# Kernel tuning notes

Hardware: AMD Instinct MI355X
Metric: run time of the kernel (lower is better)

The kernel has to match this reference:

```python
import jax, jax.numpy as jnp
import numpy as np

N = 50000
E = 800000
NODE_IN = 128
HID = 256
OUT = 256
EDGE_DIM = 16
HEADS = 4
CH = HID // HEADS  # 64
NEG_SLOPE = 0.2


def _init_linear(key, fan_in, fan_out):
    k1, k2 = jax.random.split(key)
    bound = 1.0 / np.sqrt(fan_in)
    W = jax.random.uniform(k1, (fan_in, fan_out), jnp.float32, -bound, bound)
    b = jax.random.uniform(k2, (fan_out,), jnp.float32, -bound, bound)
    return W, b


def setup_inputs() -> dict:
    key = jax.random.key(0)
    ks = jax.random.split(key, 12)
    node_feats = jax.random.normal(ks[0], (N, NODE_IN), jnp.float32)
    edge_index = jax.random.randint(ks[1], (2, E), 0, N, jnp.int64)
    edge_attr = jax.random.normal(ks[2], (E, EDGE_DIM), jnp.float32)

    Wnp, bnp = _init_linear(ks[3], NODE_IN, HID)           # node_proj
    Wep, bep = _init_linear(ks[4], EDGE_DIM, HID)          # edge_proj
    # GATConv 1: in = 2*HID, out per head = CH
    Wg1, _ = _init_linear(ks[5], 2 * HID, HEADS * CH)
    as1 = jax.random.normal(ks[6], (HEADS, CH), jnp.float32) * 0.1
    ad1 = jax.random.normal(ks[7], (HEADS, CH), jnp.float32) * 0.1
    bg1 = jnp.zeros((HEADS * CH,), jnp.float32)
    # GATConv 2: in = HID, out per head = OUT//HEADS
    Wg2, _ = _init_linear(ks[8], HID, HEADS * (OUT // HEADS))
    as2 = jax.random.normal(ks[9], (HEADS, OUT // HEADS), jnp.float32) * 0.1
    ad2 = jax.random.normal(ks[10], (HEADS, OUT // HEADS), jnp.float32) * 0.1
    bg2 = jnp.zeros((OUT,), jnp.float32)
    Wo, bo = _init_linear(ks[11], OUT, OUT)                # out_proj
    return {
        "node_feats": node_feats, "edge_attr": edge_attr,
        "Wnp": Wnp, "bnp": bnp, "Wep": Wep, "bep": bep,
        "Wg1": Wg1, "as1": as1, "ad1": ad1, "bg1": bg1,
        "Wg2": Wg2, "as2": as2, "ad2": ad2, "bg2": bg2,
        "Wo": Wo, "bo": bo,
        "edge_index": edge_index,
    }


def scatter_mean(src, index, num_nodes):
    # mean of edge features grouped by target node; empty groups -> 0 (count clamped to 1)
    s = jax.ops.segment_sum(src, index, num_segments=num_nodes)
    cnt = jax.ops.segment_sum(jnp.ones((src.shape[0],), src.dtype), index, num_segments=num_nodes)
    return s / jnp.maximum(cnt, 1.0)[:, None]


def gat_conv(x, src, dst, W, att_src, att_dst, bias, num_nodes, heads, ch):
    # PyG GATConv with add_self_loops=True (loops appended by caller via src/dst),
    # concat=True, negative_slope=0.2.
    xh = (x @ W).reshape(num_nodes, heads, ch)             # [N,H,C]
    a_src = jnp.sum(xh * att_src, axis=-1)                 # [N,H]
    a_dst = jnp.sum(xh * att_dst, axis=-1)                 # [N,H]
    logits = jax.nn.leaky_relu(a_src[src] + a_dst[dst], NEG_SLOPE)  # [E,H]
    # segment softmax over incoming edges of each destination node
    m = jax.ops.segment_max(logits, dst, num_segments=num_nodes)    # [N,H]
    ex = jnp.exp(logits - m[dst])
    denom = jax.ops.segment_sum(ex, dst, num_segments=num_nodes)    # [N,H]
    alpha = ex / denom[dst]                                          # [E,H]
    msg = xh[src] * alpha[:, :, None]                                # [E,H,C]
    out = jax.ops.segment_sum(msg, dst, num_segments=num_nodes)      # [N,H,C]
    return out.reshape(num_nodes, heads * ch) + bias


def reference(node_feats, edge_attr, Wnp, bnp, Wep, bep,
              Wg1, as1, ad1, bg1, Wg2, as2, ad2, bg2, Wo, bo, edge_index):
    n = node_feats.shape[0]
    x = node_feats @ Wnp + bnp                                       # [N,HID]
    # EdgeAggregator: mean of edge_attr over target nodes, then edge_proj
    nef = scatter_mean(edge_attr, edge_index[1], n)                  # [N,EDGE_DIM]
    nef = nef @ Wep + bep                                            # [N,HID]
    x = jnp.concatenate([x, nef], axis=-1)                           # [N,2*HID]
    # add self loops once (same augmented edge set for both GAT layers)
    loops = jnp.arange(n, dtype=edge_index.dtype)
    src = jnp.concatenate([edge_index[0], loops])
    dst = jnp.concatenate([edge_index[1], loops])
    x = jax.nn.elu(gat_conv(x, src, dst, Wg1, as1, ad1, bg1, n, HEADS, CH))
    # dropout is identity in eval mode
    x = jax.nn.elu(gat_conv(x, src, dst, Wg2, as2, ad2, bg2, n, HEADS, OUT // HEADS))
    return x @ Wo + bo
```

## Files before the change

### kernel.cpp

```cpp
#include <hip/hip_runtime.h>
#include <hip/hip_bf16.h>


#define HEADS 4

typedef __attribute__((ext_vector_type(8))) short bf16x8;
typedef __attribute__((ext_vector_type(4))) float f32x4;
typedef __attribute__((ext_vector_type(4))) unsigned short u16x4;

__device__ __forceinline__ unsigned short f2b(float v) {
    __hip_bfloat16 b = __float2bfloat16(v);
    return __builtin_bit_cast(unsigned short, b);
}
__device__ __forceinline__ float b2f(unsigned short u) {
    __hip_bfloat16 b = __builtin_bit_cast(__hip_bfloat16, u);
    return __bfloat162float(b);
}
__device__ __forceinline__ void split_hilo(float v, unsigned short& h, unsigned short& l) {
    h = f2b(v);
    l = f2b(v - b2f(h));
}
__device__ __forceinline__ unsigned short f2h(float v) {
    _Float16 h = (_Float16)v;
    return __builtin_bit_cast(unsigned short, h);
}
__device__ __forceinline__ float h2f(unsigned short u) {
    return (float)__builtin_bit_cast(_Float16, u);
}
__device__ __forceinline__ void gl2lds16(const unsigned short* g, unsigned short* l) {
    __builtin_amdgcn_global_load_lds(
        (const __attribute__((address_space(1))) unsigned int*)g,
        (__attribute__((address_space(3))) unsigned int*)l,
        16, 0, 0);
}


__global__ __launch_bounds__(256) void count_kernel(
    const int* __restrict__ dst, int* __restrict__ cnt, int E)
{
    int e = blockIdx.x * 256 + threadIdx.x;
    if (e < E) atomicAdd(&cnt[dst[e]], 1);
}

__global__ __launch_bounds__(256) void scan1_kernel(
    const int* __restrict__ cnt, int* __restrict__ chunk_sum, int N)
{
    __shared__ int sd[256];
    int t = threadIdx.x;
    int n = blockIdx.x * 256 + t;
    sd[t] = (n < N) ? (cnt[n] + 1) : 0;
    __syncthreads();
    for (int o = 128; o > 0; o >>= 1) {
        if (t < o) sd[t] += sd[t + o];
        __syncthreads();
    }
    if (t == 0) chunk_sum[blockIdx.x] = sd[0];
}

__global__ void scan2_kernel(const int* __restrict__ chunk_sum,
                             int* __restrict__ chunk_off, int nchunk)
{
    int acc = 0;
    for (int i = 0; i < nchunk; i++) {
        chunk_off[i] = acc;
        acc += chunk_sum[i];
    }
}

__global__ __launch_bounds__(256) void scan3_kernel(
    const int* __restrict__ cnt, const int* __restrict__ chunk_off,
    int* __restrict__ rowptr, int* __restrict__ fillptr,
    int* __restrict__ col, int* __restrict__ eid, int N)
{
    __shared__ int sd[256];
    int t = threadIdx.x;
    int n = blockIdx.x * 256 + t;
    int v = (n < N) ? (cnt[n] + 1) : 0;
    sd[t] = v;
    __syncthreads();
    for (int o = 1; o < 256; o <<= 1) {
        int x = (t >= o) ? sd[t - o] : 0;
        __syncthreads();
        sd[t] += x;
        __syncthreads();
    }
    if (n < N) {
        int incl = sd[t];
        int r = chunk_off[blockIdx.x] + incl - v;
        rowptr[n] = r;
        col[r] = n;
        eid[r] = -1;
        fillptr[n] = r + 1;
        if (n == N - 1) rowptr[N] = chunk_off[blockIdx.x] + incl;
    }
}

__global__ __launch_bounds__(256) void fill_kernel(
    const int* __restrict__ src, const int* __restrict__ dst,
    int* __restrict__ fillptr, int* __restrict__ col, int* __restrict__ eid, int E)
{
    int e = blockIdx.x * 256 + threadIdx.x;
    if (e >= E) return;
    int d = dst[e];
    int p = atomicAdd(&fillptr[d], 1);
    col[p] = src[e];
    eid[p] = e;
}

__global__ __launch_bounds__(256) void nef_csr_kernel(
    const float* __restrict__ ea, const int* __restrict__ rowptr,
    const int* __restrict__ eid,
    unsigned short* __restrict__ nefH, unsigned short* __restrict__ nefL, int N)
{
    int n = blockIdx.x * 4 + (threadIdx.x >> 6);
    if (n >= N) return;
    int t = threadIdx.x & 63;
    int f = t & 15, g = t >> 4;
    int base = rowptr[n], end = rowptr[n + 1];
    int deg = end - base - 1;
    float acc = 0.0f;
    for (int j = base + 1 + g; j < end; j += 4) {
        int e = eid[j];
        acc += ea[(size_t)e * 16 + f];
    }
    acc += __shfl_down(acc, 32, 64);
    acc += __shfl_down(acc, 16, 64);
    if (t < 16) {
        float v = acc / fmaxf((float)deg, 1.0f);
        unsigned short h, l;
        split_hilo(v, h, l);
        nefH[(size_t)n * 32 + t] = h;
        nefL[(size_t)n * 32 + t] = l;
    } else if (t < 32) {
        nefH[(size_t)n * 32 + t] = 0;
        nefL[(size_t)n * 32 + t] = 0;
    }
}

__global__ __launch_bounds__(256) void conv_hilo_kernel(
    const float* __restrict__ X,
    unsigned short* __restrict__ H, unsigned short* __restrict__ L, int total)
{
    int base = (blockIdx.x * 256 + threadIdx.x) * 2;
    if (base >= total) return;
    #pragma unroll
    for (int i = 0; i < 2; i++) {
        unsigned short h, l;
        split_hilo(X[base + i], h, l);
        H[base + i] = h;
        L[base + i] = l;
    }
}

__global__ __launch_bounds__(256) void pack_w_kernel(
    const float* __restrict__ W, int K, int KP,
    unsigned short* __restrict__ Ph, unsigned short* __restrict__ Pl)
{
    int idx = blockIdx.x * 256 + threadIdx.x;
    if (idx >= KP * 256) return;
    int tile = idx >> 9, w = idx & 511, lane = w >> 3, j = w & 7;
    int nk = KP >> 5;
    int ctile = tile / nk, t = tile % nk;
    int k = t * 32 + ((lane >> 4) << 3) + j;
    int n = (ctile << 4) + (lane & 15);
    float v = (k < K) ? W[(size_t)k * 256 + n] : 0.0f;
    unsigned short h, l;
    split_hilo(v, h, l);
    Ph[idx] = h;
    Pl[idx] = l;
}

template <int KSTEPS, int OMODE, bool FUSE_ATT>
__global__ __launch_bounds__(256, 4) void mfma_gemm_kernel(
    const unsigned short* __restrict__ Ah, const unsigned short* __restrict__ Al,
    int lda,
    const unsigned short* __restrict__ Ph, const unsigned short* __restrict__ Pl,
    const float* __restrict__ bias,
    float* __restrict__ Cf,
    unsigned short* __restrict__ Ch, unsigned short* __restrict__ Cl,
    int ldc, int col_off, int Nrows,
    const float* __restrict__ att_src, const float* __restrict__ att_dst,
    float* __restrict__ a_srcO, float* __restrict__ a_dstO)
{
    __shared__ unsigned short ldsB[2][2][8][512];
    int tid = threadIdx.x;
    int wave = tid >> 6, lane = tid & 63;
    int quad = lane >> 4, m16 = lane & 15;
    int rowblk = blockIdx.x, colhalf = blockIdx.y;
    int ctile0 = colhalf * 8;

    int row0 = rowblk * 128 + wave * 32 + m16;
    int row1 = row0 + 16;
    bool ok0 = row0 < Nrows, ok1 = row1 < Nrows;
    const unsigned short* arh0 = Ah + (size_t)row0 * lda;
    const unsigned short* arl0 = Al + (size_t)row0 * lda;
    const unsigned short* arh1 = Ah + (size_t)row1 * lda;
    const unsigned short* arl1 = Al + (size_t)row1 * lda;

    auto stage = [&](int t, int buf) {
        #pragma unroll
        for (int q = 0; q < 2; q++) {
            int c = wave * 2 + q;
            size_t gb = ((size_t)((ctile0 + c) * KSTEPS + t)) * 512 + lane * 8;
            gl2lds16(Ph + gb, &ldsB[buf][0][c][0]);
            gl2lds16(Pl + gb, &ldsB[buf][1][c][0]);
        }
    };

    f32x4 acc[2][8] = {};
    stage(0, 0);
    __syncthreads();

    for (int t = 0; t < KSTEPS; t++) {
        if (t + 1 < KSTEPS) stage(t + 1, (t + 1) & 1);
        int k = t * 32 + quad * 8;
        bf16x8 a_h0 = {}, a_l0 = {}, a_h1 = {}, a_l1 = {};
        if (ok0) {
            a_h0 = *(const bf16x8*)(arh0 + k);
            a_l0 = *(const bf16x8*)(arl0 + k);
        }
        if (ok1) {
            a_h1 = *(const bf16x8*)(arh1 + k);
            a_l1 = *(const bf16x8*)(arl1 + k);
        }
        int buf = t & 1;
        #pragma unroll
        for (int c = 0; c < 8; c++) {
            bf16x8 b_h = *(const bf16x8*)&ldsB[buf][0][c][lane * 8];
            bf16x8 b_l = *(const bf16x8*)&ldsB[buf][1][c][lane * 8];
            acc[0][c] = __builtin_amdgcn_mfma_f32_16x16x32_bf16(a_h0, b_h, acc[0][c], 0, 0, 0);
            acc[0][c] = __builtin_amdgcn_mfma_f32_16x16x32_bf16(a_l0, b_h, acc[0][c], 0, 0, 0);
            acc[0][c] = __builtin_amdgcn_mfma_f32_16x16x32_bf16(a_h0, b_l, acc[0][c], 0, 0, 0);
            acc[1][c] = __builtin_amdgcn_mfma_f32_16x16x32_bf16(a_h1, b_h, acc[1][c], 0, 0, 0);
            acc[1][c] = __builtin_amdgcn_mfma_f32_16x16x32_bf16(a_l1, b_h, acc[1][c], 0, 0, 0);
            acc[1][c] = __builtin_amdgcn_mfma_f32_16x16x32_bf16(a_h1, b_l, acc[1][c], 0, 0, 0);
        }
        if (t + 1 < KSTEPS) __syncthreads();
    }

    #pragma unroll
    for (int f = 0; f < 2; f++) {
        #pragma unroll
        for (int c = 0; c < 8; c++) {
            int ocol = (ctile0 + c) * 16 + m16;
            float bv = bias ? bias[ocol] : 0.0f;
            #pragma unroll
            for (int r = 0; r < 4; r++) {
                int orow = rowblk * 128 + wave * 32 + f * 16 + quad * 4 + r;
                if (orow >= Nrows) continue;
                float v = acc[f][c][r] + bv;
                size_t oidx = (size_t)orow * ldc + col_off + ocol;
                if (OMODE == 1) {
                    unsigned short h, l;
                    split_hilo(v, h, l);
                    Ch[oidx] = h;
                    Cl[oidx] = l;
                } else if (OMODE == 2) {
                    Ch[oidx] = f2h(v);
                } else {
                    Cf[oidx] = v;
                }
            }
        }
    }

    if (FUSE_ATT) {
        #pragma unroll
        for (int f = 0; f < 2; f++) {
            float ps[4][2] = {}, pd[4][2] = {};
            #pragma unroll
            for (int c = 0; c < 8; c++) {
                int ocol = (ctile0 + c) * 16 + m16;
                float asv = att_src[ocol];
                float adv = att_dst[ocol];
                int hl = c >> 2;
                #pragma unroll
                for (int r = 0; r < 4; r++) {
                    ps[r][hl] += acc[f][c][r] * asv;
                    pd[r][hl] += acc[f][c][r] * adv;
                }
            }
            #pragma unroll
            for (int r = 0; r < 4; r++) {
                #pragma unroll
                for (int hl = 0; hl < 2; hl++) {
                    float s = ps[r][hl], d = pd[r][hl];
                    #pragma unroll
                    for (int o = 8; o > 0; o >>= 1) {
                        s += __shfl_down(s, o, 64);
                        d += __shfl_down(d, o, 64);
                    }
                    if (m16 == 0) {
                        int orow = rowblk * 128 + wave * 32 + f * 16 + quad * 4 + r;
                        if (orow < Nrows) {
                            int gh = colhalf * 2 + hl;
                            a_srcO[orow * 4 + gh] = s;
                            a_dstO[orow * 4 + gh] = d;
                        }
                    }
                }
            }
        }
    }
}

__global__ __launch_bounds__(256) void gat_agg_csr_kernel(
    const unsigned short* __restrict__ xh,
    const int* __restrict__ rowptr, const int* __restrict__ col,
    const float* __restrict__ a_src, const float* __restrict__ a_dst,
    const float* __restrict__ bias,
    unsigned short* __restrict__ outH, unsigned short* __restrict__ outL, int N)
{
    int t = threadIdx.x;
    int n = blockIdx.x * 4 + (t >> 6);
    if (n >= N) return;
    int c = t & 63;
    int h = c >> 4;
    int base = rowptr[n], end = rowptr[n + 1];
    int e1 = end - 1;
    float adst = a_dst[n * 4 + h];
    const unsigned short* xcol = xh + (c << 2);

    float4 acc = {0.0f, 0.0f, 0.0f, 0.0f};
    float den = 0.0f;
    for (int j = base; j < end; j += 4) {
        int j1 = j + 1, j2 = j + 2, j3 = j + 3;
        int s0 = col[j];
        int s1 = col[j1 < e1 ? j1 : e1];
        int s2 = col[j2 < e1 ? j2 : e1];
        int s3 = col[j3 < e1 ? j3 : e1];
        float l0 = a_src[s0 * 4 + h] + adst;
        float l1 = a_src[s1 * 4 + h] + adst;
        float l2 = a_src[s2 * 4 + h] + adst;
        float l3 = a_src[s3 * 4 + h] + adst;
        l0 = fmaxf(l0, 0.2f * l0);
        l1 = fmaxf(l1, 0.2f * l1);
        l2 = fmaxf(l2, 0.2f * l2);
        l3 = fmaxf(l3, 0.2f * l3);
        float w0 = __expf(l0);
        float w1 = (j1 < end) ? __expf(l1) : 0.0f;
        float w2 = (j2 < end) ? __expf(l2) : 0.0f;
        float w3 = (j3 < end) ? __expf(l3) : 0.0f;
        u16x4 x0 = *(const u16x4*)(xcol + (size_t)s0 * 256);
        u16x4 x1 = *(const u16x4*)(xcol + (size_t)s1 * 256);
        u16x4 x2 = *(const u16x4*)(xcol + (size_t)s2 * 256);
        u16x4 x3 = *(const u16x4*)(xcol + (size_t)s3 * 256);
        den += (w0 + w1) + (w2 + w3);
        acc.x += w0 * h2f(x0[0]) + w1 * h2f(x1[0]) + w2 * h2f(x2[0]) + w3 * h2f(x3[0]);
        acc.y += w0 * h2f(x0[1]) + w1 * h2f(x1[1]) + w2 * h2f(x2[1]) + w3 * h2f(x3[1]);
        acc.z += w0 * h2f(x0[2]) + w1 * h2f(x1[2]) + w2 * h2f(x2[2]) + w3 * h2f(x3[2]);
        acc.w += w0 * h2f(x0[3]) + w1 * h2f(x1[3]) + w2 * h2f(x2[3]) + w3 * h2f(x3[3]);
    }

    float inv = 1.0f / den;
    float4 bv = *(const float4*)(bias + (c << 2));
    float o0 = acc.x * inv + bv.x;
    float o1 = acc.y * inv + bv.y;
    float o2 = acc.z * inv + bv.z;
    float o3 = acc.w * inv + bv.w;
    o0 = (o0 > 0.0f) ? o0 : (__expf(o0) - 1.0f);
    o1 = (o1 > 0.0f) ? o1 : (__expf(o1) - 1.0f);
    o2 = (o2 > 0.0f) ? o2 : (__expf(o2) - 1.0f);
    o3 = (o3 > 0.0f) ? o3 : (__expf(o3) - 1.0f);
    u16x4 H, L;
    split_hilo(o0, ((unsigned short*)&H)[0], ((unsigned short*)&L)[0]);
    split_hilo(o1, ((unsigned short*)&H)[1], ((unsigned short*)&L)[1]);
    split_hilo(o2, ((unsigned short*)&H)[2], ((unsigned short*)&L)[2]);
    split_hilo(o3, ((unsigned short*)&H)[3], ((unsigned short*)&L)[3]);
    *(u16x4*)(&outH[(size_t)n * 256 + (c << 2)]) = H;
    *(u16x4*)(&outL[(size_t)n * 256 + (c << 2)]) = L;
}


extern "C" void kernel_launch(void* const* d_in, const int* in_sizes, int n_in,
                              void* d_out, int out_size, void* d_ws, size_t ws_size,
                              hipStream_t stream)
{
    const float* node_feats = (const float*)d_in[0];
    const float* edge_attr  = (const float*)d_in[1];
    const float* Wnp = (const float*)d_in[2];
    const float* bnp = (const float*)d_in[3];
    const float* Wep = (const float*)d_in[4];
    const float* bep = (const float*)d_in[5];
    const float* Wg1 = (const float*)d_in[6];
    const float* as1 = (const float*)d_in[7];
    const float* ad1 = (const float*)d_in[8];
    const float* bg1 = (const float*)d_in[9];
    const float* Wg2 = (const float*)d_in[10];
    const float* as2 = (const float*)d_in[11];
    const float* ad2 = (const float*)d_in[12];
    const float* bg2 = (const float*)d_in[13];
    const float* Wo  = (const float*)d_in[14];
    const float* bo  = (const float*)d_in[15];
    const int*   ei  = (const int*)d_in[16];

    const int N = in_sizes[0] / 128;
    const int E = in_sizes[16] / 2;
    const int* src = ei;
    const int* dst = ei + E;
    const int nchunk = (N + 255) / 256;
    const int EN = E + N;

    typedef unsigned short u16;

    char* base = (char*)d_ws;
    size_t off = 0;
    auto alloc = [&](size_t bytes) -> char* {
        char* p = base + off;
        off += (bytes + 255) & ~(size_t)255;
        return p;
    };
    char* xreg = alloc((size_t)N * 256 * 4);
    u16* xhh  = (u16*)xreg;
    u16* x2H  = (u16*)alloc((size_t)N * 512 * 2);
    u16* x2L  = (u16*)alloc((size_t)N * 512 * 2);
    float* a_src = (float*)alloc((size_t)N * 4 * 4);
    float* a_dst = (float*)alloc((size_t)N * 4 * 4);
    u16* PnpH = (u16*)alloc(128 * 256 * 2);
    u16* PnpL = (u16*)alloc(128 * 256 * 2);
    u16* PepH = (u16*)alloc(32 * 256 * 2);
    u16* PepL = (u16*)alloc(32 * 256 * 2);
    u16* Pg1H = (u16*)alloc(512 * 256 * 2);
    u16* Pg1L = (u16*)alloc(512 * 256 * 2);
    u16* Pg2H = (u16*)alloc(256 * 256 * 2);
    u16* Pg2L = (u16*)alloc(256 * 256 * 2);
    u16* PoH  = (u16*)alloc(256 * 256 * 2);
    u16* PoL  = (u16*)alloc(256 * 256 * 2);
    int* cnt       = (int*)alloc((size_t)N * 4);
    int* rowptr    = (int*)alloc((size_t)(N + 1) * 4);
    int* fillptr   = (int*)alloc((size_t)N * 4);
    int* chunk_sum = (int*)alloc((size_t)nchunk * 4);
    int* chunk_off = (int*)alloc((size_t)nchunk * 4);
    int* colv      = (int*)alloc((size_t)EN * 4);
    int* eid       = (int*)alloc((size_t)EN * 4);

    u16* nfH  = (u16*)xreg;
    u16* nfL  = nfH + (size_t)N * 128;
    u16* nefH = nfL + (size_t)N * 128;
    u16* nefL = nefH + (size_t)N * 32;
    u16* x3H = x2H;
    u16* x3L = x2H + (size_t)N * 256;
    u16* x4H = x2L;
    u16* x4L = x2L + (size_t)N * 256;

    float* out = (float*)d_out;
    dim3 ggrid((N + 127) / 128, 2);

    hipMemsetAsync(cnt, 0, (size_t)N * sizeof(int), stream);
    count_kernel<<<(E + 255) / 256, 256, 0, stream>>>(dst, cnt, E);
    scan1_kernel<<<nchunk, 256, 0, stream>>>(cnt, chunk_sum, N);
    scan2_kernel<<<1, 1, 0, stream>>>(chunk_sum, chunk_off, nchunk);
    scan3_kernel<<<nchunk, 256, 0, stream>>>(cnt, chunk_off, rowptr, fillptr, colv, eid, N);
    fill_kernel<<<(E + 255) / 256, 256, 0, stream>>>(src, dst, fillptr, colv, eid, E);

    nef_csr_kernel<<<(N + 3) / 4, 256, 0, stream>>>(edge_attr, rowptr, eid, nefH, nefL, N);
    conv_hilo_kernel<<<((N * 128) / 2 + 255) / 256, 256, 0, stream>>>(
        node_feats, nfH, nfL, N * 128);
    pack_w_kernel<<<(128 * 256 + 255) / 256, 256, 0, stream>>>(Wnp, 128, 128, PnpH, PnpL);
    pack_w_kernel<<<(32 * 256 + 255) / 256, 256, 0, stream>>>(Wep, 16, 32, PepH, PepL);
    pack_w_kernel<<<(512 * 256 + 255) / 256, 256, 0, stream>>>(Wg1, 512, 512, Pg1H, Pg1L);
    pack_w_kernel<<<(256 * 256 + 255) / 256, 256, 0, stream>>>(Wg2, 256, 256, Pg2H, Pg2L);
    pack_w_kernel<<<(256 * 256 + 255) / 256, 256, 0, stream>>>(Wo, 256, 256, PoH, PoL);

    mfma_gemm_kernel<4, 1, false><<<ggrid, 256, 0, stream>>>(
        nfH, nfL, 128, PnpH, PnpL, bnp, nullptr, x2H, x2L, 512, 0, N,
        nullptr, nullptr, nullptr, nullptr);
    mfma_gemm_kernel<1, 1, false><<<ggrid, 256, 0, stream>>>(
        nefH, nefL, 32, PepH, PepL, bep, nullptr, x2H, x2L, 512, 256, N,
        nullptr, nullptr, nullptr, nullptr);

    mfma_gemm_kernel<16, 2, true><<<ggrid, 256, 0, stream>>>(
        x2H, x2L, 512, Pg1H, Pg1L, nullptr, nullptr, xhh, nullptr, 256, 0, N,
        as1, ad1, a_src, a_dst);
    gat_agg_csr_kernel<<<(N + 3) / 4, 256, 0, stream>>>(
        xhh, rowptr, colv, a_src, a_dst, bg1, x3H, x3L, N);

    mfma_gemm_kernel<8, 2, true><<<ggrid, 256, 0, stream>>>(
        x3H, x3L, 256, Pg2H, Pg2L, nullptr, nullptr, xhh, nullptr, 256, 0, N,
        as2, ad2, a_src, a_dst);
    gat_agg_csr_kernel<<<(N + 3) / 4, 256, 0, stream>>>(
        xhh, rowptr, colv, a_src, a_dst, bg2, x4H, x4L, N);

    mfma_gemm_kernel<8, 0, false><<<ggrid, 256, 0, stream>>>(
        x4H, x4L, 256, PoH, PoL, bo, out, nullptr, nullptr, 256, 0, N,
        nullptr, nullptr, nullptr, nullptr);
}
```

Measured before the change: 645.2 us.

## Prefetch A fragments in GEMM and precompute GAT edge weights in separate kernel

The GEMM main loop now loads the next K-step's A fragments into registers while the current step's MFMAs run. The loop is fully unrolled and the occupancy hint is lowered from 4 to 3 blocks so the extra registers fit. A new edge_w_kernel computes the per-edge attention exponentials and per-node denominators once for all four heads and stores them to a buffer. The aggregation kernel then reads these weights instead of recomputing leaky-relu and exp per channel lane. This removes redundant exp work and gathered a_src reads, at the cost of an extra launch and writing and reading an edge-sized weight buffer.

```diff
diff --git a/kernel.cpp b/kernel.cpp
--- a/kernel.cpp
+++ b/kernel.cpp
@@ -171,7 +171,7 @@
 }
 
 template <int KSTEPS, int OMODE, bool FUSE_ATT>
-__global__ __launch_bounds__(256, 4) void mfma_gemm_kernel(
+__global__ __launch_bounds__(256, 3) void mfma_gemm_kernel(
     const unsigned short* __restrict__ Ah, const unsigned short* __restrict__ Al,
     int lda,
     const unsigned short* __restrict__ Ph, const unsigned short* __restrict__ Pl,
@@ -206,36 +206,47 @@
             gl2lds16(Pl + gb, &ldsB[buf][1][c][0]);
         }
     };
+    auto loadA = [&](int t, bf16x8& h0, bf16x8& l0, bf16x8& h1, bf16x8& l1) {
+        int k = t * 32 + quad * 8;
+        h0 = l0 = h1 = l1 = (bf16x8){};
+        if (ok0) {
+            h0 = *(const bf16x8*)(arh0 + k);
+            l0 = *(const bf16x8*)(arl0 + k);
+        }
+        if (ok1) {
+            h1 = *(const bf16x8*)(arh1 + k);
+            l1 = *(const bf16x8*)(arl1 + k);
+        }
+    };
 
     f32x4 acc[2][8] = {};
+    bf16x8 cah0, cal0, cah1, cal1, nah0, nal0, nah1, nal1;
+    loadA(0, cah0, cal0, cah1, cal1);
     stage(0, 0);
     __syncthreads();
 
+    #pragma unroll
     for (int t = 0; t < KSTEPS; t++) {
-        if (t + 1 < KSTEPS) stage(t + 1, (t + 1) & 1);
-        int k = t * 32 + quad * 8;
-        bf16x8 a_h0 = {}, a_l0 = {}, a_h1 = {}, a_l1 = {};
-        if (ok0) {
-            a_h0 = *(const bf16x8*)(arh0 + k);
-            a_l0 = *(const bf16x8*)(arl0 + k);
-        }
-        if (ok1) {
-            a_h1 = *(const bf16x8*)(arh1 + k);
-            a_l1 = *(const bf16x8*)(arl1 + k);
-        }
-        int buf = t & 1;
+        const int buf = t & 1;
+        if (t + 1 < KSTEPS) {
+            stage(t + 1, buf ^ 1);
+            loadA(t + 1, nah0, nal0, nah1, nal1);
+        }
         #pragma unroll
         for (int c = 0; c < 8; c++) {
             bf16x8 b_h = *(const bf16x8*)&ldsB[buf][0][c][lane * 8];
             bf16x8 b_l = *(const bf16x8*)&ldsB[buf][1][c][lane * 8];
-            acc[0][c] = __builtin_amdgcn_mfma_f32_16x16x32_bf16(a_h0, b_h, acc[0][c], 0, 0, 0);
-            acc[0][c] = __builtin_amdgcn_mfma_f32_16x16x32_bf16(a_l0, b_h, acc[0][c], 0, 0, 0);
-            acc[0][c] = __builtin_amdgcn_mfma_f32_16x16x32_bf16(a_h0, b_l, acc[0][c], 0, 0, 0);
-            acc[1][c] = __builtin_amdgcn_mfma_f32_16x16x32_bf16(a_h1, b_h, acc[1][c], 0, 0, 0);
-            acc[1][c] = __builtin_amdgcn_mfma_f32_16x16x32_bf16(a_l1, b_h, acc[1][c], 0, 0, 0);
-            acc[1][c] = __builtin_amdgcn_mfma_f32_16x16x32_bf16(a_h1, b_l, acc[1][c], 0, 0, 0);
-        }
-        if (t + 1 < KSTEPS) __syncthreads();
+            acc[0][c] = __builtin_amdgcn_mfma_f32_16x16x32_bf16(cah0, b_h, acc[0][c], 0, 0, 0);
+            acc[0][c] = __builtin_amdgcn_mfma_f32_16x16x32_bf16(cal0, b_h, acc[0][c], 0, 0, 0);
+            acc[0][c] = __builtin_amdgcn_mfma_f32_16x16x32_bf16(cah0, b_l, acc[0][c], 0, 0, 0);
+            acc[1][c] = __builtin_amdgcn_mfma_f32_16x16x32_bf16(cah1, b_h, acc[1][c], 0, 0, 0);
+            acc[1][c] = __builtin_amdgcn_mfma_f32_16x16x32_bf16(cal1, b_h, acc[1][c], 0, 0, 0);
+            acc[1][c] = __builtin_amdgcn_mfma_f32_16x16x32_bf16(cah1, b_l, acc[1][c], 0, 0, 0);
+        }
+        if (t + 1 < KSTEPS) {
+            __syncthreads();
+            cah0 = nah0; cal0 = nal0; cah1 = nah1; cal1 = nal1;
+        }
     }
 
     #pragma unroll
@@ -304,10 +315,44 @@
     }
 }
 
+__global__ __launch_bounds__(256) void edge_w_kernel(
+    const int* __restrict__ rowptr, const int* __restrict__ col,
+    const float* __restrict__ a_src, const float* __restrict__ a_dst,
+    float* __restrict__ wq, float* __restrict__ den, int N)
+{
+    int n = blockIdx.x * 4 + (threadIdx.x >> 6);
+    if (n >= N) return;
+    int lane = threadIdx.x & 63;
+    int base = rowptr[n], end = rowptr[n + 1];
+    float4 ad = *(const float4*)&a_dst[n * 4];
+    float4 ds = {0.0f, 0.0f, 0.0f, 0.0f};
+    for (int j = base + lane; j < end; j += 64) {
+        int s = col[j];
+        float4 as4 = *(const float4*)&a_src[s * 4];
+        float l0 = as4.x + ad.x, l1 = as4.y + ad.y;
+        float l2 = as4.z + ad.z, l3 = as4.w + ad.w;
+        l0 = fmaxf(l0, 0.2f * l0);
+        l1 = fmaxf(l1, 0.2f * l1);
+        l2 = fmaxf(l2, 0.2f * l2);
+        l3 = fmaxf(l3, 0.2f * l3);
+        float4 wv = {__expf(l0), __expf(l1), __expf(l2), __expf(l3)};
+        *(float4*)&wq[(size_t)j * 4] = wv;
+        ds.x += wv.x; ds.y += wv.y; ds.z += wv.z; ds.w += wv.w;
+    }
+    #pragma unroll
+    for (int o = 32; o > 0; o >>= 1) {
+        ds.x += __shfl_down(ds.x, o, 64);
+        ds.y += __shfl_down(ds.y, o, 64);
+        ds.z += __shfl_down(ds.z, o, 64);
+        ds.w += __shfl_down(ds.w, o, 64);
+    }
+    if (lane == 0) *(float4*)&den[n * 4] = ds;
+}
+
 __global__ __launch_bounds__(256) void gat_agg_csr_kernel(
     const unsigned short* __restrict__ xh,
     const int* __restrict__ rowptr, const int* __restrict__ col,
-    const float* __restrict__ a_src, const float* __restrict__ a_dst,
+    const float* __restrict__ wq, const float* __restrict__ den,
     const float* __restrict__ bias,
     unsigned short* __restrict__ outH, unsigned short* __restrict__ outL, int N)
 {
@@ -318,41 +363,29 @@
     int h = c >> 4;
     int base = rowptr[n], end = rowptr[n + 1];
     int e1 = end - 1;
-    float adst = a_dst[n * 4 + h];
+    float inv = 1.0f / den[n * 4 + h];
     const unsigned short* xcol = xh + (c << 2);
 
     float4 acc = {0.0f, 0.0f, 0.0f, 0.0f};
-    float den = 0.0f;
     for (int j = base; j < end; j += 4) {
-        int j1 = j + 1, j2 = j + 2, j3 = j + 3;
-        int s0 = col[j];
-        int s1 = col[j1 < e1 ? j1 : e1];
-        int s2 = col[j2 < e1 ? j2 : e1];
-        int s3 = col[j3 < e1 ? j3 : e1];
-        float l0 = a_src[s0 * 4 + h] + adst;
-        float l1 = a_src[s1 * 4 + h] + adst;
-        float l2 = a_src[s2 * 4 + h] + adst;
-        float l3 = a_src[s3 * 4 + h] + adst;
-        l0 = fmaxf(l0, 0.2f * l0);
-        l1 = fmaxf(l1, 0.2f * l1);
-        l2 = fmaxf(l2, 0.2f * l2);
-        l3 = fmaxf(l3, 0.2f * l3);
-        float w0 = __expf(l0);
-        float w1 = (j1 < end) ? __expf(l1) : 0.0f;
-        float w2 = (j2 < end) ? __expf(l2) : 0.0f;
-        float w3 = (j3 < end) ? __expf(l3) : 0.0f;
+        int j1 = j + 1 < e1 ? j + 1 : e1;
+        int j2 = j + 2 < e1 ? j + 2 : e1;
+        int j3 = j + 3 < e1 ? j + 3 : e1;
+        int s0 = col[j], s1 = col[j1], s2 = col[j2], s3 = col[j3];
+        float w0 = wq[(size_t)j * 4 + h];
+        float w1 = (j + 1 < end) ? wq[(size_t)j1 * 4 + h] : 0.0f;
+        float w2 = (j + 2 < end) ? wq[(size_t)j2 * 4 + h] : 0.0f;
+        float w3 = (j + 3 < end) ? wq[(size_t)j3 * 4 + h] : 0.0f;
         u16x4 x0 = *(const u16x4*)(xcol + (size_t)s0 * 256);
         u16x4 x1 = *(const u16x4*)(xcol + (size_t)s1 * 256);
         u16x4 x2 = *(const u16x4*)(xcol + (size_t)s2 * 256);
         u16x4 x3 = *(const u16x4*)(xcol + (size_t)s3 * 256);
-        den += (w0 + w1) + (w2 + w3);
         acc.x += w0 * h2f(x0[0]) + w1 * h2f(x1[0]) + w2 * h2f(x2[0]) + w3 * h2f(x3[0]);
         acc.y += w0 * h2f(x0[1]) + w1 * h2f(x1[1]) + w2 * h2f(x2[1]) + w3 * h2f(x3[1]);
         acc.z += w0 * h2f(x0[2]) + w1 * h2f(x1[2]) + w2 * h2f(x2[2]) + w3 * h2f(x3[2]);
         acc.w += w0 * h2f(x0[3]) + w1 * h2f(x1[3]) + w2 * h2f(x2[3]) + w3 * h2f(x3[3]);
     }
 
-    float inv = 1.0f / den;
     float4 bv = *(const float4*)(bias + (c << 2));
     float o0 = acc.x * inv + bv.x;
     float o1 = acc.y * inv + bv.y;
@@ -416,6 +449,8 @@
     u16* x2L  = (u16*)alloc((size_t)N * 512 * 2);
     float* a_src = (float*)alloc((size_t)N * 4 * 4);
     float* a_dst = (float*)alloc((size_t)N * 4 * 4);
+    float* wq    = (float*)alloc((size_t)EN * 4 * 4);
+    float* den   = (float*)alloc((size_t)N * 4 * 4);
     u16* PnpH = (u16*)alloc(128 * 256 * 2);
     u16* PnpL = (u16*)alloc(128 * 256 * 2);
     u16* PepH = (u16*)alloc(32 * 256 * 2);
@@ -472,14 +507,18 @@
     mfma_gemm_kernel<16, 2, true><<<ggrid, 256, 0, stream>>>(
         x2H, x2L, 512, Pg1H, Pg1L, nullptr, nullptr, xhh, nullptr, 256, 0, N,
         as1, ad1, a_src, a_dst);
+    edge_w_kernel<<<(N + 3) / 4, 256, 0, stream>>>(
+        rowptr, colv, a_src, a_dst, wq, den, N);
     gat_agg_csr_kernel<<<(N + 3) / 4, 256, 0, stream>>>(
-        xhh, rowptr, colv, a_src, a_dst, bg1, x3H, x3L, N);
+        xhh, rowptr, colv, wq, den, bg1, x3H, x3L, N);
 
     mfma_gemm_kernel<8, 2, true><<<ggrid, 256, 0, stream>>>(
         x3H, x3L, 256, Pg2H, Pg2L, nullptr, nullptr, xhh, nullptr, 256, 0, N,
         as2, ad2, a_src, a_dst);
+    edge_w_kernel<<<(N + 3) / 4, 256, 0, stream>>>(
+        rowptr, colv, a_src, a_dst, wq, den, N);
     gat_agg_csr_kernel<<<(N + 3) / 4, 256, 0, stream>>>(
-        xhh, rowptr, colv, a_src, a_dst, bg2, x4H, x4L, N);
+        xhh, rowptr, colv, wq, den, bg2, x4H, x4L, N);
 
     mfma_gemm_kernel<8, 0, false><<<ggrid, 256, 0, stream>>>(
         x4H, x4L, 256, PoH, PoL, bo, out, nullptr, nullptr, 256, 0, N,
```

Measured after the change: 692.9 us. 7.4% more time.
